# Kernel optimization log

Measured on AMD Instinct MI355X. Metric: run time of the kernel, lower is better.

## Reference

```python
import jax, jax.numpy as jnp
import numpy as np

DIM_MODEL = 512
INV_SCALE = DIM_MODEL ** (-0.5)  # NOTE: source DIVIDES by this, i.e. multiplies scores by sqrt(d)


def setup_inputs() -> dict:
    key = jax.random.key(0)
    ks = jax.random.split(key, 9)
    B, LQ, LKV, D = 32, 64, 4096, DIM_MODEL
    lim = 1.0 / np.sqrt(D)  # torch Linear default init range
    return {
        "x1": jax.random.normal(ks[0], (B, LQ, D), dtype=jnp.float32),
        "x2": jax.random.normal(ks[1], (B, LKV, D), dtype=jnp.float32),
        "mask": jnp.zeros((B, LQ, LKV), dtype=bool),
        "wq": jax.random.uniform(ks[2], (D, D), jnp.float32, -lim, lim),
        "bq": jax.random.uniform(ks[3], (D,), jnp.float32, -lim, lim),
        "wk": jax.random.uniform(ks[4], (D, D), jnp.float32, -lim, lim),
        "bk": jax.random.uniform(ks[5], (D,), jnp.float32, -lim, lim),
        "wv": jax.random.uniform(ks[6], (D, D), jnp.float32, -lim, lim),
        "bv": jax.random.uniform(ks[7], (D,), jnp.float32, -lim, lim),
    }


def reference(x1, x2, mask, wq, bq, wk, bk, wv, bv):
    # torch.nn.Linear: y = x @ W^T + b
    q = jnp.einsum("bqd,ed->bqe", x1, wq) + bq          # [B, LQ, D]
    k = jnp.einsum("bkd,ed->bke", x2, wk) + bk          # [B, LKV, D]
    v = jnp.einsum("bkd,ed->bke", x2, wv) + bv          # [B, LKV, D]
    qk = jnp.einsum("bqd,bkd->bqk", q, k)               # [B, LQ, LKV]
    scaled_qk = qk / INV_SCALE                           # faithful: divide by d^-0.5
    p = jax.nn.softmax(scaled_qk, axis=-1)
    # dropout p=0.0 -> identity; mask is unused in the original forward
    return jnp.einsum("bqk,bkd->bqd", p, v)              # [B, LQ, D]
```

## Files before the change

### kernel.cpp

```cpp
#include <hip/hip_runtime.h>
#include <math.h>


#define LQ 64
#define LKV 4096
#define NB 32
#define DM 512
#define SCALE 22.627416997969522f
#define KEYS_TOTAL (NB * LKV)
#define NCHUNK 16
#define CHUNK 256
#define PBS 264

typedef __attribute__((ext_vector_type(8))) short bf16x8;
typedef __attribute__((ext_vector_type(4))) float f32x4;
typedef __attribute__((ext_vector_type(8))) unsigned short u16x8;
typedef __attribute__((ext_vector_type(4))) unsigned short u16x4;

__device__ __forceinline__ unsigned short f2bf(float f) {
    unsigned u = __float_as_uint(f);
    u += 0x7fffu + ((u >> 16) & 1u);
    return (unsigned short)(u >> 16);
}
__device__ __forceinline__ float bf2f(unsigned short s) {
    return __uint_as_float(((unsigned)s) << 16);
}
__device__ __forceinline__ void gld16(const void* g, void* l) {
    __builtin_amdgcn_global_load_lds(
        (const __attribute__((address_space(1))) unsigned int*)g,
        (__attribute__((address_space(3))) unsigned int*)l, 16, 0, 0);
}

__global__ __launch_bounds__(256) void split_kernel(const float* __restrict__ src,
                                                    unsigned short* __restrict__ hi,
                                                    unsigned short* __restrict__ lo) {
    size_t idx = ((size_t)blockIdx.x * 256 + threadIdx.x) * 8;
    float4 a = *(const float4*)(src + idx);
    float4 b = *(const float4*)(src + idx + 4);
    float ff[8] = {a.x, a.y, a.z, a.w, b.x, b.y, b.z, b.w};
    u16x8 h, l;
#pragma unroll
    for (int i = 0; i < 8; ++i) {
        h[i] = f2bf(ff[i]);
        l[i] = f2bf(ff[i] - bf2f(h[i]));
    }
    *(u16x8*)(hi + idx) = h;
    *(u16x8*)(lo + idx) = l;
}

__global__ __launch_bounds__(256) void transpose_kernel(const float* __restrict__ in,
                                                        float* __restrict__ outT) {
    __shared__ float T[64 * 65];
    const int bx = blockIdx.x * 64, by = blockIdx.y * 64;
    const int t = threadIdx.x, col = t & 63, rg = t >> 6;
#pragma unroll
    for (int i = 0; i < 16; ++i) {
        int row = i * 4 + rg;
        T[col * 65 + row] = in[(size_t)(by + row) * DM + bx + col];
    }
    __syncthreads();
#pragma unroll
    for (int i = 0; i < 16; ++i) {
        int row = i * 4 + rg;
        outT[(size_t)(bx + row) * DM + by + col] = T[row * 65 + col];
    }
}

__global__ __launch_bounds__(256) void bmfold_kernel(const float* __restrict__ bq,
                                                     const float* __restrict__ wk,
                                                     float* __restrict__ bM) {
    int d = blockIdx.x * 256 + threadIdx.x;
    float s = 0.f;
#pragma unroll 8
    for (int e = 0; e < 512; ++e) s = fmaf(bq[e], wk[(size_t)e * DM + d], s);
    bM[d] = s;
}

__global__ __launch_bounds__(256) void sgemm_kernel(
        const unsigned short* __restrict__ Ah_g, const unsigned short* __restrict__ Al_g,
        const unsigned short* __restrict__ Bh_g, const unsigned short* __restrict__ Bl_g,
        const float* __restrict__ bias, int mode,
        unsigned short* __restrict__ out0, unsigned short* __restrict__ out2l,
        float* __restrict__ outf) {
    __shared__ unsigned short smem[16384];
    unsigned short* Ah = smem;
    unsigned short* Al = smem + 4096;
    unsigned short* Bh = smem + 8192;
    unsigned short* Bl = smem + 12288;

    const int bn = blockIdx.x, bm = blockIdx.y;
    const int t = threadIdx.x, w = t >> 6, l = t & 63;
    const int wm = (w >> 1) * 64, wn = (w & 1) * 64;
    const int c16 = l & 15, q = l >> 4, q8 = q << 3;
    const int rB = l >> 2, cB = (l & 3) << 3;

    f32x4 acc[4][4];
#pragma unroll
    for (int i = 0; i < 4; ++i)
#pragma unroll
        for (int jj = 0; jj < 4; ++jj) acc[i][jj] = (f32x4){0.f,0.f,0.f,0.f};

    for (int k0 = 0; k0 < DM; k0 += 32) {
#pragma unroll
        for (int jj = 0; jj < 2; ++jj) {
            int r = w * 32 + jj * 16;
            size_t ga = (size_t)(bm * 128 + r + rB) * DM + k0 + cB;
            gld16(Ah_g + ga, &Ah[r * 32]);
            gld16(Al_g + ga, &Al[r * 32]);
            size_t gb = (size_t)(bn * 128 + r + rB) * DM + k0 + cB;
            gld16(Bh_g + gb, &Bh[r * 32]);
            gld16(Bl_g + gb, &Bl[r * 32]);
        }
        __syncthreads();
        bf16x8 ah[4], al[4];
#pragma unroll
        for (int mt = 0; mt < 4; ++mt) {
            ah[mt] = *(const bf16x8*)&Ah[(wm + mt*16 + c16) * 32 + q8];
            al[mt] = *(const bf16x8*)&Al[(wm + mt*16 + c16) * 32 + q8];
        }
#pragma unroll
        for (int nt = 0; nt < 4; ++nt) {
            bf16x8 bh = *(const bf16x8*)&Bh[(wn + nt*16 + c16) * 32 + q8];
            bf16x8 bl = *(const bf16x8*)&Bl[(wn + nt*16 + c16) * 32 + q8];
#pragma unroll
            for (int mt = 0; mt < 4; ++mt) {
                acc[mt][nt] = __builtin_amdgcn_mfma_f32_16x16x32_bf16(ah[mt], bh, acc[mt][nt], 0, 0, 0);
                acc[mt][nt] = __builtin_amdgcn_mfma_f32_16x16x32_bf16(al[mt], bh, acc[mt][nt], 0, 0, 0);
                acc[mt][nt] = __builtin_amdgcn_mfma_f32_16x16x32_bf16(ah[mt], bl, acc[mt][nt], 0, 0, 0);
            }
        }
        __syncthreads();
    }

#pragma unroll
    for (int mt = 0; mt < 4; ++mt)
#pragma unroll
        for (int nt = 0; nt < 4; ++nt) {
            int col = bn * 128 + wn + nt * 16 + c16;
            float bia = bias ? bias[col] : 0.f;
#pragma unroll
            for (int r = 0; r < 4; ++r) {
                size_t row = (size_t)bm * 128 + wm + mt * 16 + q * 4 + r;
                float y = acc[mt][nt][r] + bia;
                if (mode == 0) {
                    unsigned short h = f2bf(y);
                    out0[row * 1024 + col]       = h;
                    out0[row * 1024 + 512 + col] = f2bf(y - bf2f(h));
                } else if (mode == 1) {
                    outf[row * 512 + col] = y;
                } else {
                    unsigned short h = f2bf(y);
                    out0[row * 512 + col]  = h;
                    out2l[row * 512 + col] = f2bf(y - bf2f(h));
                }
            }
        }
}

__global__ __launch_bounds__(256) void splitT_kernel(const float* __restrict__ src,
        unsigned short* __restrict__ x2m, unsigned short* __restrict__ x2ht) {
    __shared__ unsigned short T[128 * 136];
    const int d0 = blockIdx.x * 128, k0 = blockIdx.y * 128;
    const int t = threadIdx.x;
    const int cg = t & 31, rg = t >> 5;
#pragma unroll
    for (int i = 0; i < 16; ++i) {
        int row = i * 8 + rg;
        float4 v = *(const float4*)(src + (size_t)(k0 + row) * DM + d0 + cg * 4);
        float ff[4] = {v.x, v.y, v.z, v.w};
        u16x4 h, lo_;
#pragma unroll
        for (int j = 0; j < 4; ++j) {
            h[j]   = f2bf(ff[j]);
            lo_[j] = f2bf(ff[j] - bf2f(h[j]));
        }
        size_t gm = (size_t)(k0 + row) * 1024 + d0 + cg * 4;
        *(u16x4*)(x2m + gm)       = h;
        *(u16x4*)(x2m + gm + 512) = lo_;
        int rsw = row ^ ((cg & 15) << 3);
#pragma unroll
        for (int j = 0; j < 4; ++j)
            T[(cg * 4 + j) * 136 + rsw] = h[j];
    }
    __syncthreads();
#pragma unroll
    for (int ii = 0; ii < 8; ++ii) {
        int dl = ii * 16 + (t >> 4);
        int ko = (t & 15) * 8;
        u16x8 vv = *(const u16x8*)&T[dl * 136 + (ko ^ (((dl >> 2) & 15) << 3))];
        *(u16x8*)(x2ht + (size_t)(d0 + dl) * KEYS_TOTAL + k0 + ko) = vv;
    }
}

__global__ __launch_bounds__(512, 4) void attn_kernel(
        const unsigned short* __restrict__ Q2,
        const unsigned short* __restrict__ K2,
        const unsigned short* __restrict__ Vt,
        float* __restrict__ Opart,
        float* __restrict__ ML) {
    __shared__ char smem_raw[69120];
    unsigned short* Qh = (unsigned short*)smem_raw;
    unsigned short* Ql = (unsigned short*)(smem_raw + 4096);
    unsigned short* Kh = (unsigned short*)(smem_raw + 8192);
    unsigned short* Kl = (unsigned short*)(smem_raw + 24576);
    unsigned short* Pb = (unsigned short*)smem_raw;
    unsigned short* Vb = (unsigned short*)(smem_raw + 33792);
    float* redb = (float*)(smem_raw + 66560);
    float* mrow = (float*)(smem_raw + 68608);
    float* lrow = (float*)(smem_raw + 68864);

    const int c = blockIdx.x, b = blockIdx.y;
    const int t = threadIdx.x, w = t >> 6, l = t & 63;
    const int c16 = l & 15, q = l >> 4, q8 = q << 3;
    const int rB = l >> 2, cB = (l & 3) << 3;
    const size_t key0 = (size_t)b * LKV + (size_t)c * CHUNK;

    f32x4 acc[4][2];
#pragma unroll
    for (int i = 0; i < 4; ++i)
#pragma unroll
        for (int jj = 0; jj < 2; ++jj) acc[i][jj] = (f32x4){0.f,0.f,0.f,0.f};

    for (int k0 = 0; k0 < DM; k0 += 32) {
        if (w < 4)
            gld16(Q2 + (size_t)(b * 64 + w * 16 + rB) * 1024 + k0 + cB, &Qh[(w * 16) * 32]);
        else
            gld16(Q2 + (size_t)(b * 64 + (w - 4) * 16 + rB) * 1024 + 512 + k0 + cB, &Ql[((w - 4) * 16) * 32]);
#pragma unroll
        for (int jj = 0; jj < 2; ++jj) {
            int r = w * 32 + jj * 16;
            size_t krow = key0 + r + rB;
            gld16(K2 + krow * 1024 + k0 + cB,       &Kh[r * 32]);
            gld16(K2 + krow * 1024 + 512 + k0 + cB, &Kl[r * 32]);
        }
        __syncthreads();
        bf16x8 ah[4], al[4];
#pragma unroll
        for (int mt = 0; mt < 4; ++mt) {
            ah[mt] = *(const bf16x8*)&Qh[(mt * 16 + c16) * 32 + q8];
            al[mt] = *(const bf16x8*)&Ql[(mt * 16 + c16) * 32 + q8];
        }
#pragma unroll
        for (int nt = 0; nt < 2; ++nt) {
            bf16x8 bh = *(const bf16x8*)&Kh[(w * 32 + nt * 16 + c16) * 32 + q8];
            bf16x8 bl = *(const bf16x8*)&Kl[(w * 32 + nt * 16 + c16) * 32 + q8];
#pragma unroll
            for (int mt = 0; mt < 4; ++mt) {
                acc[mt][nt] = __builtin_amdgcn_mfma_f32_16x16x32_bf16(ah[mt], bh, acc[mt][nt], 0, 0, 0);
                acc[mt][nt] = __builtin_amdgcn_mfma_f32_16x16x32_bf16(al[mt], bh, acc[mt][nt], 0, 0, 0);
                acc[mt][nt] = __builtin_amdgcn_mfma_f32_16x16x32_bf16(ah[mt], bl, acc[mt][nt], 0, 0, 0);
            }
        }
        __syncthreads();
    }

#pragma unroll
    for (int mt = 0; mt < 4; ++mt)
#pragma unroll
        for (int nt = 0; nt < 2; ++nt)
#pragma unroll
            for (int r = 0; r < 4; ++r) acc[mt][nt][r] *= SCALE;

    float rmax_[4][4];
#pragma unroll
    for (int mt = 0; mt < 4; ++mt)
#pragma unroll
        for (int r = 0; r < 4; ++r)
            rmax_[mt][r] = fmaxf(acc[mt][0][r], acc[mt][1][r]);
#pragma unroll
    for (int off = 1; off < 16; off <<= 1)
#pragma unroll
        for (int mt = 0; mt < 4; ++mt)
#pragma unroll
            for (int r = 0; r < 4; ++r)
                rmax_[mt][r] = fmaxf(rmax_[mt][r], __shfl_xor(rmax_[mt][r], off));
    if (c16 == 0) {
#pragma unroll
        for (int mt = 0; mt < 4; ++mt)
#pragma unroll
            for (int r = 0; r < 4; ++r) redb[w * 64 + mt * 16 + q * 4 + r] = rmax_[mt][r];
    }
    __syncthreads();
    if (t < 64) {
        float m = redb[t];
#pragma unroll
        for (int ww = 1; ww < 8; ++ww) m = fmaxf(m, redb[ww * 64 + t]);
        mrow[t] = m;
    }
    __syncthreads();

    float rsum_[4][4];
#pragma unroll
    for (int mt = 0; mt < 4; ++mt)
#pragma unroll
        for (int r = 0; r < 4; ++r) {
            float m = mrow[mt * 16 + q * 4 + r];
            float s = 0.f;
#pragma unroll
            for (int nt = 0; nt < 2; ++nt) {
                float e = __expf(acc[mt][nt][r] - m);
                acc[mt][nt][r] = e;
                s += e;
            }
            rsum_[mt][r] = s;
        }
#pragma unroll
    for (int off = 1; off < 16; off <<= 1)
#pragma unroll
        for (int mt = 0; mt < 4; ++mt)
#pragma unroll
            for (int r = 0; r < 4; ++r) rsum_[mt][r] += __shfl_xor(rsum_[mt][r], off);
    if (c16 == 0) {
#pragma unroll
        for (int mt = 0; mt < 4; ++mt)
#pragma unroll
            for (int r = 0; r < 4; ++r) redb[w * 64 + mt * 16 + q * 4 + r] = rsum_[mt][r];
    }
    __syncthreads();
    if (t < 64) {
        float s = redb[t];
#pragma unroll
        for (int ww = 1; ww < 8; ++ww) s += redb[ww * 64 + t];
        lrow[t] = s;
    }
#pragma unroll
    for (int mt = 0; mt < 4; ++mt)
#pragma unroll
        for (int nt = 0; nt < 2; ++nt)
#pragma unroll
            for (int r = 0; r < 4; ++r)
                Pb[(mt * 16 + q * 4 + r) * PBS + w * 32 + nt * 16 + c16] = f2bf(acc[mt][nt][r]);
    __syncthreads();

    f32x4 accO[4][4];
#pragma unroll
    for (int i = 0; i < 4; ++i)
#pragma unroll
        for (int jj = 0; jj < 4; ++jj) accO[i][jj] = (f32x4){0.f,0.f,0.f,0.f};

    for (int ks = 0; ks < CHUNK; ks += 32) {
#pragma unroll
        for (int jj = 0; jj < 4; ++jj) {
            int d = jj * 128 + w * 16;
            gld16(Vt + (size_t)(d + rB) * KEYS_TOTAL + key0 + ks + cB, &Vb[d * 32]);
        }
        __syncthreads();
        bf16x8 ap[4];
#pragma unroll
        for (int mt = 0; mt < 4; ++mt)
            ap[mt] = *(const bf16x8*)&Pb[(mt * 16 + c16) * PBS + ks + q8];
#pragma unroll
        for (int nt = 0; nt < 4; ++nt) {
            bf16x8 bv = *(const bf16x8*)&Vb[(w * 64 + nt * 16 + c16) * 32 + q8];
#pragma unroll
            for (int mt = 0; mt < 4; ++mt)
                accO[mt][nt] = __builtin_amdgcn_mfma_f32_16x16x32_bf16(ap[mt], bv, accO[mt][nt], 0, 0, 0);
        }
        __syncthreads();
    }

    const size_t part = (size_t)b * NCHUNK + c;
#pragma unroll
    for (int mt = 0; mt < 4; ++mt)
#pragma unroll
        for (int nt = 0; nt < 4; ++nt)
#pragma unroll
            for (int r = 0; r < 4; ++r)
                Opart[(part * 64 + mt * 16 + q * 4 + r) * 512 + w * 64 + nt * 16 + c16] = accO[mt][nt][r];
    if (t < 64) {
        ML[part * 128 + t]      = mrow[t];
        ML[part * 128 + 64 + t] = lrow[t];
    }
}

__global__ __launch_bounds__(128) void combine_kernel(const float* __restrict__ Opart,
                                                      const float* __restrict__ ML,
                                                      unsigned short* __restrict__ Uh,
                                                      unsigned short* __restrict__ Ul) {
    const int b = blockIdx.x >> 6, row = blockIdx.x & 63;
    const int t = threadIdx.x;
    float m[NCHUNK], lv[NCHUNK];
    float M = -1e30f;
#pragma unroll
    for (int c = 0; c < NCHUNK; ++c) {
        m[c]  = ML[(size_t)(b * NCHUNK + c) * 128 + row];
        lv[c] = ML[(size_t)(b * NCHUNK + c) * 128 + 64 + row];
        M = fmaxf(M, m[c]);
    }
    float den = 0.f, wgt[NCHUNK];
#pragma unroll
    for (int c = 0; c < NCHUNK; ++c) { wgt[c] = __expf(m[c] - M); den += wgt[c] * lv[c]; }
    float4 o = make_float4(0.f, 0.f, 0.f, 0.f);
#pragma unroll
    for (int c = 0; c < NCHUNK; ++c) {
        float4 v = *(const float4*)&Opart[((size_t)(b * NCHUNK + c) * 64 + row) * 512 + t * 4];
        o.x += wgt[c] * v.x; o.y += wgt[c] * v.y; o.z += wgt[c] * v.z; o.w += wgt[c] * v.w;
    }
    const float inv = 1.f / den;
    float rr[4] = {o.x * inv, o.y * inv, o.z * inv, o.w * inv};
    u16x4 h, lo_;
#pragma unroll
    for (int j = 0; j < 4; ++j) {
        h[j]   = f2bf(rr[j]);
        lo_[j] = f2bf(rr[j] - bf2f(h[j]));
    }
    size_t base = ((size_t)(b * 64 + row)) * 512 + t * 4;
    *(u16x4*)&Uh[base] = h;
    *(u16x4*)&Ul[base] = lo_;
}

extern "C" void kernel_launch(void* const* d_in, const int* in_sizes, int n_in,
                              void* d_out, int out_size, void* d_ws, size_t ws_size,
                              hipStream_t stream) {
    const float* x1 = (const float*)d_in[0];
    const float* x2 = (const float*)d_in[1];
    const float* wq = (const float*)d_in[3];
    const float* bq = (const float*)d_in[4];
    const float* wk = (const float*)d_in[5];
    const float* wv = (const float*)d_in[7];
    const float* bv = (const float*)d_in[8];
    float* out = (float*)d_out;

    char* ws = (char*)d_ws;
    unsigned short* x2m   = (unsigned short*)(ws);
    unsigned short* x2ht  = (unsigned short*)(ws + 268435456);
    float*          Opart = (float*)(ws + 402653184);
    float*          ML    = (float*)(ws + 469762048);
    unsigned short* M2    = (unsigned short*)(ws + 470024192);
    unsigned short* x1h   = (unsigned short*)(ws + 474218496);
    unsigned short* x1l   = (unsigned short*)(ws + 476315648);
    unsigned short* Uh    = (unsigned short*)(ws + 478412800);
    unsigned short* Ul    = (unsigned short*)(ws + 480509952);
    float*          Wqt   = (float*)(ws + 482607104);
    float*          Wkt   = (float*)(ws + 483655680);
    unsigned short* wqth  = (unsigned short*)(ws + 484704256);
    unsigned short* wqtl  = (unsigned short*)(ws + 485228544);
    unsigned short* wkth  = (unsigned short*)(ws + 485752832);
    unsigned short* wktl  = (unsigned short*)(ws + 486277120);
    unsigned short* wvh   = (unsigned short*)(ws + 486801408);
    unsigned short* wvl   = (unsigned short*)(ws + 487325696);
    unsigned short* WMTh  = (unsigned short*)(ws + 487849984);
    unsigned short* WMTl  = (unsigned short*)(ws + 488374272);
    float*          bM    = (float*)(ws + 488898560);

    splitT_kernel<<<dim3(4, 1024), 256, 0, stream>>>(x2, x2m, x2ht);

    transpose_kernel<<<dim3(8, 8), 256, 0, stream>>>(wq, Wqt);
    transpose_kernel<<<dim3(8, 8), 256, 0, stream>>>(wk, Wkt);
    bmfold_kernel<<<2, 256, 0, stream>>>(bq, wk, bM);
    split_kernel<<<128, 256, 0, stream>>>(Wqt, wqth, wqtl);
    split_kernel<<<128, 256, 0, stream>>>(Wkt, wkth, wktl);
    split_kernel<<<128, 256, 0, stream>>>(wv, wvh, wvl);
    split_kernel<<<512, 256, 0, stream>>>(x1, x1h, x1l);
    sgemm_kernel<<<dim3(4, 4), 256, 0, stream>>>(wkth, wktl, wqth, wqtl,
                                                 nullptr, 2, WMTh, WMTl, nullptr);
    sgemm_kernel<<<dim3(4, 16), 256, 0, stream>>>(x1h, x1l, WMTh, WMTl,
                                                  bM, 0, M2, nullptr, nullptr);

    attn_kernel<<<dim3(NCHUNK, NB), 512, 0, stream>>>(M2, x2m, x2ht, Opart, ML);
    combine_kernel<<<NB * LQ, 128, 0, stream>>>(Opart, ML, Uh, Ul);

    sgemm_kernel<<<dim3(4, 16), 256, 0, stream>>>(Uh, Ul, wvh, wvl,
                                                  bv, 1, nullptr, nullptr, out);
}
```

Measured before the change: 697.9 us.

## Double-buffer QK and PV LDS staging and compute Q projection before folding Wk

The attention kernel now double-buffers its Q/K tiles and V tiles in shared memory, issuing the next tile's loads before computing the current one. This removes one barrier per iteration and lets global loads overlap the MFMA work. PV is split into two passes over halves of the output columns, and LDS use grows to 80KB, which may lower occupancy. The preprocessing also changes order: it computes q = x1·Wq^T + bq first and then q·Wk, fusing transpose and split, instead of forming Wk^T·Wq^T and a folded bias. That drops several small kernels.

```diff
diff --git a/kernel.cpp b/kernel.cpp
--- a/kernel.cpp
+++ b/kernel.cpp
@@ -48,8 +48,8 @@
     *(u16x8*)(lo + idx) = l;
 }
 
-__global__ __launch_bounds__(256) void transpose_kernel(const float* __restrict__ in,
-                                                        float* __restrict__ outT) {
+__global__ __launch_bounds__(256) void transposeSplit_kernel(const float* __restrict__ in,
+        unsigned short* __restrict__ hi, unsigned short* __restrict__ lo) {
     __shared__ float T[64 * 65];
     const int bx = blockIdx.x * 64, by = blockIdx.y * 64;
     const int t = threadIdx.x, col = t & 63, rg = t >> 6;
@@ -62,18 +62,11 @@
 #pragma unroll
     for (int i = 0; i < 16; ++i) {
         int row = i * 4 + rg;
-        outT[(size_t)(bx + row) * DM + by + col] = T[row * 65 + col];
-    }
-}
-
-__global__ __launch_bounds__(256) void bmfold_kernel(const float* __restrict__ bq,
-                                                     const float* __restrict__ wk,
-                                                     float* __restrict__ bM) {
-    int d = blockIdx.x * 256 + threadIdx.x;
-    float s = 0.f;
-#pragma unroll 8
-    for (int e = 0; e < 512; ++e) s = fmaf(bq[e], wk[(size_t)e * DM + d], s);
-    bM[d] = s;
+        float v = T[row * 65 + col];
+        unsigned short h = f2bf(v);
+        hi[(size_t)(bx + row) * DM + by + col] = h;
+        lo[(size_t)(bx + row) * DM + by + col] = f2bf(v - bf2f(h));
+    }
 }
 
 __global__ __launch_bounds__(256) void sgemm_kernel(
@@ -198,13 +191,8 @@
         const unsigned short* __restrict__ Vt,
         float* __restrict__ Opart,
         float* __restrict__ ML) {
-    __shared__ char smem_raw[69120];
-    unsigned short* Qh = (unsigned short*)smem_raw;
-    unsigned short* Ql = (unsigned short*)(smem_raw + 4096);
-    unsigned short* Kh = (unsigned short*)(smem_raw + 8192);
-    unsigned short* Kl = (unsigned short*)(smem_raw + 24576);
+    __shared__ char smem_raw[81920];
     unsigned short* Pb = (unsigned short*)smem_raw;
-    unsigned short* Vb = (unsigned short*)(smem_raw + 33792);
     float* redb = (float*)(smem_raw + 66560);
     float* mrow = (float*)(smem_raw + 68608);
     float* lrow = (float*)(smem_raw + 68864);
@@ -221,7 +209,12 @@
 #pragma unroll
         for (int jj = 0; jj < 2; ++jj) acc[i][jj] = (f32x4){0.f,0.f,0.f,0.f};
 
-    for (int k0 = 0; k0 < DM; k0 += 32) {
+    auto stageQK = [&](int s, int k0) {
+        char* base = smem_raw + s * 40960;
+        unsigned short* Qh = (unsigned short*)base;
+        unsigned short* Ql = (unsigned short*)(base + 4096);
+        unsigned short* Kh = (unsigned short*)(base + 8192);
+        unsigned short* Kl = (unsigned short*)(base + 24576);
         if (w < 4)
             gld16(Q2 + (size_t)(b * 64 + w * 16 + rB) * 1024 + k0 + cB, &Qh[(w * 16) * 32]);
         else
@@ -233,7 +226,18 @@
             gld16(K2 + krow * 1024 + k0 + cB,       &Kh[r * 32]);
             gld16(K2 + krow * 1024 + 512 + k0 + cB, &Kl[r * 32]);
         }
-        __syncthreads();
+    };
+
+    stageQK(0, 0);
+    __syncthreads();
+#pragma unroll 1
+    for (int k0 = 0; k0 < DM; k0 += 32) {
+        const int s = (k0 >> 5) & 1;
+        if (k0 + 32 < DM) stageQK(s ^ 1, k0 + 32);
+        const unsigned short* Qh = (const unsigned short*)(smem_raw + s * 40960);
+        const unsigned short* Ql = Qh + 2048;
+        const unsigned short* Kh = Qh + 4096;
+        const unsigned short* Kl = Qh + 12288;
         bf16x8 ah[4], al[4];
 #pragma unroll
         for (int mt = 0; mt < 4; ++mt) {
@@ -253,6 +257,17 @@
         }
         __syncthreads();
     }
+
+    auto stagePV = [&](int s, int h, int ks) {
+        unsigned short* Vb = (unsigned short*)(smem_raw + 33792 + s * 16384);
+#pragma unroll
+        for (int jj = 0; jj < 2; ++jj) {
+            int dloc = w * 32 + jj * 16;
+            gld16(Vt + (size_t)(h * 256 + dloc + rB) * KEYS_TOTAL + key0 + ks * 32 + cB,
+                  &Vb[dloc * 32]);
+        }
+    };
+    stagePV(0, 0, 0);
 
 #pragma unroll
     for (int mt = 0; mt < 4; ++mt)
@@ -338,23 +353,40 @@
 #pragma unroll
         for (int jj = 0; jj < 4; ++jj) accO[i][jj] = (f32x4){0.f,0.f,0.f,0.f};
 
-    for (int ks = 0; ks < CHUNK; ks += 32) {
-#pragma unroll
-        for (int jj = 0; jj < 4; ++jj) {
-            int d = jj * 128 + w * 16;
-            gld16(Vt + (size_t)(d + rB) * KEYS_TOTAL + key0 + ks + cB, &Vb[d * 32]);
+#pragma unroll 1
+    for (int ks = 0; ks < 8; ++ks) {
+        const int s = ks & 1;
+        if (ks < 7) stagePV(s ^ 1, 0, ks + 1);
+        else        stagePV(s ^ 1, 1, 0);
+        const unsigned short* Vb = (const unsigned short*)(smem_raw + 33792 + s * 16384);
+        bf16x8 ap[4];
+#pragma unroll
+        for (int mt = 0; mt < 4; ++mt)
+            ap[mt] = *(const bf16x8*)&Pb[(mt * 16 + c16) * PBS + ks * 32 + q8];
+#pragma unroll
+        for (int nt = 0; nt < 2; ++nt) {
+            bf16x8 bvv = *(const bf16x8*)&Vb[(w * 32 + nt * 16 + c16) * 32 + q8];
+#pragma unroll
+            for (int mt = 0; mt < 4; ++mt)
+                accO[mt][nt] = __builtin_amdgcn_mfma_f32_16x16x32_bf16(ap[mt], bvv, accO[mt][nt], 0, 0, 0);
         }
         __syncthreads();
+    }
+#pragma unroll 1
+    for (int ks = 0; ks < 8; ++ks) {
+        const int s = ks & 1;
+        if (ks < 7) stagePV(s ^ 1, 1, ks + 1);
+        const unsigned short* Vb = (const unsigned short*)(smem_raw + 33792 + s * 16384);
         bf16x8 ap[4];
 #pragma unroll
         for (int mt = 0; mt < 4; ++mt)
-            ap[mt] = *(const bf16x8*)&Pb[(mt * 16 + c16) * PBS + ks + q8];
-#pragma unroll
-        for (int nt = 0; nt < 4; ++nt) {
-            bf16x8 bv = *(const bf16x8*)&Vb[(w * 64 + nt * 16 + c16) * 32 + q8];
+            ap[mt] = *(const bf16x8*)&Pb[(mt * 16 + c16) * PBS + ks * 32 + q8];
+#pragma unroll
+        for (int nt = 0; nt < 2; ++nt) {
+            bf16x8 bvv = *(const bf16x8*)&Vb[(w * 32 + nt * 16 + c16) * 32 + q8];
 #pragma unroll
             for (int mt = 0; mt < 4; ++mt)
-                accO[mt][nt] = __builtin_amdgcn_mfma_f32_16x16x32_bf16(ap[mt], bv, accO[mt][nt], 0, 0, 0);
+                accO[mt][2 + nt] = __builtin_amdgcn_mfma_f32_16x16x32_bf16(ap[mt], bvv, accO[mt][2 + nt], 0, 0, 0);
         }
         __syncthreads();
     }
@@ -363,10 +395,14 @@
 #pragma unroll
     for (int mt = 0; mt < 4; ++mt)
 #pragma unroll
-        for (int nt = 0; nt < 4; ++nt)
-#pragma unroll
-            for (int r = 0; r < 4; ++r)
-                Opart[(part * 64 + mt * 16 + q * 4 + r) * 512 + w * 64 + nt * 16 + c16] = accO[mt][nt][r];
+        for (int h = 0; h < 2; ++h)
+#pragma unroll
+            for (int nt = 0; nt < 2; ++nt) {
+                int col = h * 256 + w * 32 + nt * 16 + c16;
+#pragma unroll
+                for (int r = 0; r < 4; ++r)
+                    Opart[(part * 64 + mt * 16 + q * 4 + r) * 512 + col] = accO[mt][h * 2 + nt][r];
+            }
     if (t < 64) {
         ML[part * 128 + t]      = mrow[t];
         ML[part * 128 + 64 + t] = lrow[t];
@@ -431,31 +467,25 @@
     unsigned short* x1l   = (unsigned short*)(ws + 476315648);
     unsigned short* Uh    = (unsigned short*)(ws + 478412800);
     unsigned short* Ul    = (unsigned short*)(ws + 480509952);
-    float*          Wqt   = (float*)(ws + 482607104);
-    float*          Wkt   = (float*)(ws + 483655680);
-    unsigned short* wqth  = (unsigned short*)(ws + 484704256);
-    unsigned short* wqtl  = (unsigned short*)(ws + 485228544);
-    unsigned short* wkth  = (unsigned short*)(ws + 485752832);
-    unsigned short* wktl  = (unsigned short*)(ws + 486277120);
-    unsigned short* wvh   = (unsigned short*)(ws + 486801408);
-    unsigned short* wvl   = (unsigned short*)(ws + 487325696);
-    unsigned short* WMTh  = (unsigned short*)(ws + 487849984);
-    unsigned short* WMTl  = (unsigned short*)(ws + 488374272);
-    float*          bM    = (float*)(ws + 488898560);
+    unsigned short* q1h   = (unsigned short*)(ws + 482607104);
+    unsigned short* q1l   = (unsigned short*)(ws + 484704256);
+    unsigned short* wqh   = (unsigned short*)(ws + 486801408);
+    unsigned short* wql   = (unsigned short*)(ws + 487325696);
+    unsigned short* wkth  = (unsigned short*)(ws + 487849984);
+    unsigned short* wktl  = (unsigned short*)(ws + 488374272);
+    unsigned short* wvh   = (unsigned short*)(ws + 488898560);
+    unsigned short* wvl   = (unsigned short*)(ws + 489422848);
 
     splitT_kernel<<<dim3(4, 1024), 256, 0, stream>>>(x2, x2m, x2ht);
 
-    transpose_kernel<<<dim3(8, 8), 256, 0, stream>>>(wq, Wqt);
-    transpose_kernel<<<dim3(8, 8), 256, 0, stream>>>(wk, Wkt);
-    bmfold_kernel<<<2, 256, 0, stream>>>(bq, wk, bM);
-    split_kernel<<<128, 256, 0, stream>>>(Wqt, wqth, wqtl);
-    split_kernel<<<128, 256, 0, stream>>>(Wkt, wkth, wktl);
+    split_kernel<<<512, 256, 0, stream>>>(x1, x1h, x1l);
+    split_kernel<<<128, 256, 0, stream>>>(wq, wqh, wql);
+    transposeSplit_kernel<<<dim3(8, 8), 256, 0, stream>>>(wk, wkth, wktl);
     split_kernel<<<128, 256, 0, stream>>>(wv, wvh, wvl);
-    split_kernel<<<512, 256, 0, stream>>>(x1, x1h, x1l);
-    sgemm_kernel<<<dim3(4, 4), 256, 0, stream>>>(wkth, wktl, wqth, wqtl,
-                                                 nullptr, 2, WMTh, WMTl, nullptr);
-    sgemm_kernel<<<dim3(4, 16), 256, 0, stream>>>(x1h, x1l, WMTh, WMTl,
-                                                  bM, 0, M2, nullptr, nullptr);
+    sgemm_kernel<<<dim3(4, 16), 256, 0, stream>>>(x1h, x1l, wqh, wql,
+                                                  bq, 2, q1h, q1l, nullptr);
+    sgemm_kernel<<<dim3(4, 16), 256, 0, stream>>>(q1h, q1l, wkth, wktl,
+                                                  nullptr, 0, M2, nullptr, nullptr);
 
     attn_kernel<<<dim3(NCHUNK, NB), 512, 0, stream>>>(M2, x2m, x2ht, Opart, ML);
     combine_kernel<<<NB * LQ, 128, 0, stream>>>(Opart, ML, Uh, Ul);
```

After: 663.3 us. 5.0% less time.
